# Optimization experiments

Hardware: AMD Instinct MI355X
Metric: run time of the kernel (lower is better)

## Reference

```python
import jax, jax.numpy as jnp
import numpy as np

B, K, P, N, COEF_D = 32, 2, 256, 8192, 10  # batch, parts, kp-per-part, cloud points
BETA = 0.1
SEP_FACTOR = 8.0
W_CHF, W_COV, W_SURF, W_JOINT, W_REG, W_SEP = 1.0, 1.0, 5.0, 1.0, 0.01, 2.0
# separation-loss pair indices (static, same as torch buffers select1/select2)
SEL1 = np.tile(np.arange(P), P - 1)
SEL2 = np.concatenate([np.arange(j, j + P) % P for j in range(1, P)])


def _pdist(a, b):
    # a: (..., M, 3), b: (..., N, 3) -> (..., M, N) euclidean distances
    d2 = (jnp.sum(a * a, -1)[..., :, None] + jnp.sum(b * b, -1)[..., None, :]
          - 2.0 * jnp.einsum('...mc,...nc->...mn', a, b))
    return jnp.sqrt(jnp.maximum(d2, 1e-12))


def _smooth_l1(pred, target, beta=BETA):
    d = jnp.abs(pred - target)
    return jnp.where(d < beta, 0.5 * d * d / beta, d - 0.5 * beta)


def setup_inputs() -> dict:
    key = jax.random.key(0)
    ks = jax.random.split(key, 10)
    return {
        'coefs': jax.random.normal(ks[0], (B, K * P, COEF_D), jnp.float32),
        'part_pred_kps': jax.random.normal(ks[1], (B, K, P, 3), jnp.float32),
        'part_nodes': jax.random.normal(ks[2], (B, K, P, 3), jnp.float32),
        'cloud': jax.random.normal(ks[3], (B, N, 3), jnp.float32),
        'cloud_cls': jax.random.randint(ks[4], (B, N), 0, K, jnp.int64),
        'pred_joint_loc': jax.random.normal(ks[5], (B, K - 1, 3), jnp.float32),
        'pred_joint_axis': jax.random.normal(ks[6], (B, K - 1, 3), jnp.float32),
        'gt_joint_loc': jax.random.normal(ks[7], (B, K - 1, 3), jnp.float32),
        'gt_joint_axis': jax.random.normal(ks[8], (B, K - 1, 3), jnp.float32),
        'gt_part_scale': jax.random.uniform(ks[9], (B, K, 3), jnp.float32),
    }


def _forward(coefs, part_pred_kps, part_nodes, cloud,
             pred_joint_loc, pred_joint_axis, gt_joint_loc, gt_joint_axis,
             gt_part_scale, cloud_cls):
    # ---- part chamfer (brute) over all parts at once: (B,K,M,N) ----
    d_chf = _pdist(part_pred_kps, part_nodes)
    fwd = jnp.min(d_chf, axis=3).mean(axis=(0, 2))   # (K,)
    bwd = jnp.min(d_chf, axis=2).mean(axis=(0, 2))   # (K,)
    chf_loss = jnp.mean(fwd + bwd)

    # ---- coverage loss: masked per-part pc extremes vs node extremes ----
    mask = cloud_cls[:, None, :] == jnp.arange(K)[None, :, None]  # (B,K,N)
    big = jnp.float32(1e9)
    pc = cloud[:, None, :, :]                                      # (B,1,N,3)
    pc_max = jnp.max(jnp.where(mask[..., None], pc, -big), axis=2)  # (B,K,3)
    pc_min = jnp.min(jnp.where(mask[..., None], pc, big), axis=2)
    kp_max = jnp.max(part_nodes, axis=2)                            # (B,K,3)
    kp_min = jnp.min(part_nodes, axis=2)
    cov_loss = jnp.mean((_smooth_l1(kp_max, pc_max) + _smooth_l1(kp_min, pc_min)) * 0.5)

    # ---- separation loss ----
    a = part_nodes[:, :, SEL1, :]
    b = part_nodes[:, :, SEL2, :]
    dist_sep = jnp.linalg.norm(a - b, axis=-1)                      # (B,K,L)
    thr = (jnp.linalg.norm(gt_part_scale, axis=-1) / SEP_FACTOR)[:, :, None]
    sep_loss = jnp.mean(jnp.maximum(0.0, thr - dist_sep))

    # ---- surface loss: single-side chamfer nodes -> cloud ----
    nodes = part_nodes.reshape(B, K * P, 3)
    d_surf = _pdist(nodes, cloud)                                   # (B, K*P, N)
    surf_loss = jnp.min(d_surf, axis=2).mean()

    # ---- joint loss ----
    dot = jnp.sum(pred_joint_axis * gt_joint_axis, -1)
    na = jnp.linalg.norm(pred_joint_axis, axis=-1)
    nb = jnp.linalg.norm(gt_joint_axis, axis=-1)
    loss_axis = 1.0 - (dot / jnp.maximum(na * nb, 1e-8)).mean()
    ngt = gt_joint_axis / jnp.linalg.norm(gt_joint_axis, axis=-1, keepdims=True)
    p = gt_joint_loc
    q = gt_joint_loc + ngt
    r = pred_joint_loc
    x = p - q
    t = jnp.sum((r - q) * x, -1, keepdims=True) / jnp.sum(x * x, -1, keepdims=True)
    loss_loc = jnp.linalg.norm(t * (p - q) + (q - r), axis=-1).mean()
    joint_loss = loss_loc * 1.0 + loss_axis * 0.5  # revolute: loc_weight=1, axis_weight=0.5

    reg_loss = jnp.mean(coefs * coefs)

    return (chf_loss * W_CHF + cov_loss * W_COV + surf_loss * W_SURF
            + joint_loss * W_JOINT + reg_loss * W_REG + sep_loss * W_SEP)


def reference(coefs, part_pred_kps, part_nodes, cloud, cloud_cls,
              pred_joint_loc, pred_joint_axis, gt_joint_loc, gt_joint_axis,
              gt_part_scale):
    return _forward(coefs, part_pred_kps, part_nodes, cloud,
                    pred_joint_loc, pred_joint_axis, gt_joint_loc,
                    gt_joint_axis, gt_part_scale, cloud_cls)
```

## Files before the change

kernel.cpp:

```cpp
#include <hip/hip_runtime.h>
#include <math.h>

#define NB 32
#define KK 2
#define PP 256
#define NCLOUD 8192
#define NNODES 512
#define NCOEF 163840
#define SURF0 193
#define NCHUNK 16
#define NSURF (NB * NCHUNK)
#define NBLK (SURF0 + NSURF)

#define SL_CHF 0
#define SL_SEP 64
#define SL_COV 128
#define SL_REG 192
#define SL_JNT 256
#define SL_SB 258
#define PART0 320

__device__ inline float waveSum(float v) {
#pragma unroll
  for (int o = 32; o > 0; o >>= 1) v += __shfl_down(v, o);
  return v;
}
__device__ inline float waveMax(float v) {
#pragma unroll
  for (int o = 32; o > 0; o >>= 1) v = fmaxf(v, __shfl_down(v, o));
  return v;
}
__device__ inline float waveMin(float v) {
#pragma unroll
  for (int o = 32; o > 0; o >>= 1) v = fminf(v, __shfl_down(v, o));
  return v;
}
__device__ inline float smooth_l1(float d) {
  d = fabsf(d);
  return d < 0.1f ? 5.0f * d * d : d - 0.05f;
}

__global__ __launch_bounds__(256) void mega_kernel(
    const float* __restrict__ coefs,
    const float* __restrict__ preds,
    const float* __restrict__ nodes,
    const float* __restrict__ cloud,
    const int* __restrict__ cls,
    const float* __restrict__ pjl, const float* __restrict__ pja,
    const float* __restrict__ gjl, const float* __restrict__ gja,
    const float* __restrict__ gps,
    float* __restrict__ ws) {
  const int bid = blockIdx.x;
  const int t = threadIdx.x;
  const int wave = t >> 6, lane = t & 63;
  __shared__ float4 sh4[512];
  __shared__ float shg[2048];
  __shared__ float red[12][4];

  if (bid < 64) {
    const int bk = bid;
    const float* pb = preds + (size_t)bk * PP * 3;
    const float* nbp = nodes + (size_t)bk * PP * 3;
    {
      float x = pb[3 * t], y = pb[3 * t + 1], z = pb[3 * t + 2];
      sh4[t] = make_float4(x, y, z, x * x + y * y + z * z);
      x = nbp[3 * t]; y = nbp[3 * t + 1]; z = nbp[3 * t + 2];
      sh4[256 + t] = make_float4(x, y, z, x * x + y * y + z * z);
    }
    __syncthreads();
    float4 ptv[4], ntv[4];
#pragma unroll
    for (int q = 0; q < 4; ++q) {
      ptv[q] = sh4[lane + q * 64];
      ntv[q] = sh4[256 + lane + q * 64];
    }
    const float s0 = gps[bk * 3 + 0], s1 = gps[bk * 3 + 1], s2 = gps[bk * 3 + 2];
    const float thr = sqrtf(s0 * s0 + s1 * s1 + s2 * s2) * 0.125f;
    float g1[4], g2[4], sep = 0.0f;
#pragma unroll
    for (int q = 0; q < 4; ++q) { g1[q] = 1e30f; g2[q] = 1e30f; }
    const int j0 = wave * 64;
#pragma unroll 2
    for (int jj = 0; jj < 64; ++jj) {
      const int j = j0 + jj;
      const float4 pj = sh4[j];
      const float4 nj = sh4[256 + j];
#pragma unroll
      for (int q = 0; q < 4; ++q) {
        float dot = fmaf(ptv[q].x, nj.x, fmaf(ptv[q].y, nj.y, ptv[q].z * nj.z));
        g1[q] = fminf(g1[q], fmaf(-2.0f, dot, nj.w));
        dot = fmaf(ntv[q].x, pj.x, fmaf(ntv[q].y, pj.y, ntv[q].z * pj.z));
        g2[q] = fminf(g2[q], fmaf(-2.0f, dot, pj.w));
        dot = fmaf(ntv[q].x, nj.x, fmaf(ntv[q].y, nj.y, ntv[q].z * nj.z));
        const float d2 = fmaf(-2.0f, dot, ntv[q].w + nj.w);
        const float d = sqrtf(fmaxf(d2, 0.0f));
        if (j != lane + q * 64) sep += fmaxf(thr - d, 0.0f);
      }
    }
#pragma unroll
    for (int q = 0; q < 4; ++q) {
      shg[wave * 256 + lane + q * 64] = g1[q];
      shg[1024 + wave * 256 + lane + q * 64] = g2[q];
    }
    __syncthreads();
    const float gf = fminf(fminf(shg[t], shg[256 + t]),
                           fminf(shg[512 + t], shg[768 + t]));
    const float gb = fminf(fminf(shg[1024 + t], shg[1280 + t]),
                           fminf(shg[1536 + t], shg[1792 + t]));
    float chf = sqrtf(fmaxf(sh4[t].w + gf, 1e-12f)) +
                sqrtf(fmaxf(sh4[256 + t].w + gb, 1e-12f));
    chf = waveSum(chf);
    sep = waveSum(sep);
    if (lane == 0) { red[0][wave] = chf; red[1][wave] = sep; }
    __syncthreads();
    if (t == 0) {
      ws[SL_CHF + bid] = red[0][0] + red[0][1] + red[0][2] + red[0][3];
      ws[SL_SEP + bid] = red[1][0] + red[1][1] + red[1][2] + red[1][3];
    }

  } else if (bid < 128) {
    const int bk = bid - 64;
    const int b = bk >> 1;
    const int k = bk & 1;
    float pmax0 = -1e9f, pmax1 = -1e9f, pmax2 = -1e9f;
    float pmin0 = 1e9f, pmin1 = 1e9f, pmin2 = 1e9f;
    const float* cb = cloud + (size_t)b * NCLOUD * 3;
    const int* lb = cls + (size_t)b * NCLOUD;
    for (int i = t; i < NCLOUD; i += 256) {
      if (lb[i] == k) {
        const float x = cb[i * 3 + 0], y = cb[i * 3 + 1], z = cb[i * 3 + 2];
        pmax0 = fmaxf(pmax0, x); pmax1 = fmaxf(pmax1, y); pmax2 = fmaxf(pmax2, z);
        pmin0 = fminf(pmin0, x); pmin1 = fminf(pmin1, y); pmin2 = fminf(pmin2, z);
      }
    }
    const float* nb = nodes + (size_t)bk * PP * 3;
    const float kx = nb[t * 3 + 0], ky = nb[t * 3 + 1], kz = nb[t * 3 + 2];
    pmax0 = waveMax(pmax0); pmax1 = waveMax(pmax1); pmax2 = waveMax(pmax2);
    pmin0 = waveMin(pmin0); pmin1 = waveMin(pmin1); pmin2 = waveMin(pmin2);
    float kmax0 = waveMax(kx), kmax1 = waveMax(ky), kmax2 = waveMax(kz);
    float kmin0 = waveMin(kx), kmin1 = waveMin(ky), kmin2 = waveMin(kz);
    if (lane == 0) {
      red[0][wave] = pmax0; red[1][wave] = pmax1; red[2][wave] = pmax2;
      red[3][wave] = pmin0; red[4][wave] = pmin1; red[5][wave] = pmin2;
      red[6][wave] = kmax0; red[7][wave] = kmax1; red[8][wave] = kmax2;
      red[9][wave] = kmin0; red[10][wave] = kmin1; red[11][wave] = kmin2;
    }
    __syncthreads();
    if (t == 0) {
      float v[12];
#pragma unroll
      for (int q = 0; q < 12; ++q) {
        if (q < 3 || (q >= 6 && q < 9))
          v[q] = fmaxf(fmaxf(red[q][0], red[q][1]), fmaxf(red[q][2], red[q][3]));
        else
          v[q] = fminf(fminf(red[q][0], red[q][1]), fminf(red[q][2], red[q][3]));
      }
      float s = 0.0f;
#pragma unroll
      for (int c2 = 0; c2 < 3; ++c2)
        s += 0.5f * (smooth_l1(v[6 + c2] - v[0 + c2]) + smooth_l1(v[9 + c2] - v[3 + c2]));
      ws[SL_COV + bk] = s;
    }

  } else if (bid < 192) {
    const int r = bid - 128;
    const float4* c4 = (const float4*)coefs;
    float v = 0.0f;
    for (int i = r * 256 + t; i < NCOEF / 4; i += 64 * 256) {
      const float4 q = c4[i];
      v += q.x * q.x + q.y * q.y + q.z * q.z + q.w * q.w;
    }
    v = waveSum(v);
    if (lane == 0) red[0][wave] = v;
    __syncthreads();
    if (t == 0)
      ws[SL_REG + r] = red[0][0] + red[0][1] + red[0][2] + red[0][3];

  } else if (bid == 192) {
    float cosv = 0.0f, locv = 0.0f;
    if (t < NB) {
      const float axj = pja[t * 3 + 0], ayj = pja[t * 3 + 1], azj = pja[t * 3 + 2];
      const float gx = gja[t * 3 + 0], gy = gja[t * 3 + 1], gz = gja[t * 3 + 2];
      const float dot = axj * gx + ayj * gy + azj * gz;
      const float na = sqrtf(axj * axj + ayj * ayj + azj * azj);
      const float nbn = sqrtf(gx * gx + gy * gy + gz * gz);
      cosv = dot / fmaxf(na * nbn, 1e-8f);
      const float ux = gx / nbn, uy = gy / nbn, uz = gz / nbn;
      const float px = gjl[t * 3 + 0], py = gjl[t * 3 + 1], pz = gjl[t * 3 + 2];
      const float qx = px + ux, qy = py + uy, qz = pz + uz;
      const float rx = pjl[t * 3 + 0], ry = pjl[t * 3 + 1], rz = pjl[t * 3 + 2];
      const float xx = px - qx, xy = py - qy, xz = pz - qz;
      const float tnum = (rx - qx) * xx + (ry - qy) * xy + (rz - qz) * xz;
      const float tden = xx * xx + xy * xy + xz * xz;
      const float tv = tnum / tden;
      const float vx = tv * xx + (qx - rx);
      const float vy = tv * xy + (qy - ry);
      const float vz = tv * xz + (qz - rz);
      locv = sqrtf(vx * vx + vy * vy + vz * vz);
    }
    cosv = waveSum(cosv);
    locv = waveSum(locv);
    if (t == 0) { ws[SL_JNT + 0] = cosv; ws[SL_JNT + 1] = locv; }

  } else {
    const int s = bid - SURF0;
    const int b = s >> 4;
    const int c = s & 15;
    const float* cb = cloud + ((size_t)b * NCLOUD + (size_t)c * 512) * 3;
#pragma unroll
    for (int g = 0; g < 2; ++g) {
      const int idx = g * 256 + t;
      const float qx = cb[3 * idx], qy = cb[3 * idx + 1], qz = cb[3 * idx + 2];
      sh4[idx] = make_float4(qx, qy, qz, 0.5f * (qx * qx + qy * qy + qz * qz));
    }
    __syncthreads();
    const float* nb = nodes + (size_t)b * NNODES * 3;
    float nxv[8], nyv[8], nzv[8], mg[8];
#pragma unroll
    for (int q = 0; q < 8; ++q) {
      const int n = lane + q * 64;
      nxv[q] = nb[3 * n]; nyv[q] = nb[3 * n + 1]; nzv[q] = nb[3 * n + 2];
      mg[q] = 1e30f;
    }
    const int p0 = wave * 128;
#pragma unroll 4
    for (int j = 0; j < 128; ++j) {
      const float4 q4 = sh4[p0 + j];
#pragma unroll
      for (int q = 0; q < 8; ++q)
        mg[q] = fminf(mg[q],
                      fmaf(-nxv[q], q4.x,
                           fmaf(-nyv[q], q4.y, fmaf(-nzv[q], q4.z, q4.w))));
    }
#pragma unroll
    for (int q = 0; q < 8; ++q)
      shg[wave * 512 + lane + q * 64] = mg[q];
    __syncthreads();
    float* pout = ws + PART0 + ((size_t)b * NCHUNK + c) * NNODES;
#pragma unroll
    for (int g = 0; g < 2; ++g) {
      const int node = g * 256 + t;
      pout[node] = fminf(fminf(shg[node], shg[512 + node]),
                         fminf(shg[1024 + node], shg[1536 + node]));
    }
  }
}

__global__ __launch_bounds__(256) void final1_kernel(
    const float* __restrict__ nodes, float* __restrict__ ws) {
  const int b = blockIdx.x;
  const int t = threadIdx.x;
  const float* partial = ws + PART0;
  const float* nb = nodes + (size_t)b * NNODES * 3;
  float ssum = 0.0f;
#pragma unroll
  for (int g = 0; g < 2; ++g) {
    const int node = g * 256 + t;
    float m = 1e30f;
#pragma unroll
    for (int c = 0; c < NCHUNK; ++c)
      m = fminf(m, partial[((size_t)b * NCHUNK + c) * NNODES + node]);
    const float x = nb[3 * node], y = nb[3 * node + 1], z = nb[3 * node + 2];
    const float nn = x * x + y * y + z * z;
    ssum += sqrtf(fmaxf(fmaf(2.0f, m, nn), 1e-12f));
  }
  ssum = waveSum(ssum);
  __shared__ float r[4];
  const int wave = t >> 6, lane = t & 63;
  if (lane == 0) r[wave] = ssum;
  __syncthreads();
  if (t == 0) ws[SL_SB + b] = r[0] + r[1] + r[2] + r[3];
}

__global__ __launch_bounds__(64) void final2_kernel(
    const float* __restrict__ ws, float* __restrict__ out) {
  const int t = threadIdx.x;
  float chf_s = ws[SL_CHF + t];
  float sep_s = ws[SL_SEP + t];
  float cov_s = ws[SL_COV + t];
  float reg_s = ws[SL_REG + t];
  float srf_s = (t < NB) ? ws[SL_SB + t] : 0.0f;
  chf_s = waveSum(chf_s);
  sep_s = waveSum(sep_s);
  cov_s = waveSum(cov_s);
  reg_s = waveSum(reg_s);
  srf_s = waveSum(srf_s);
  if (t == 0) {
    const float chf = chf_s / (float)(KK * NB * PP);
    const float sep = sep_s / (float)(NB * KK * PP * (PP - 1));
    const float surf = srf_s / (float)(NB * NNODES);
    const float cov = cov_s / (float)(NB * KK * 3);
    const float axis = 1.0f - ws[SL_JNT + 0] / (float)NB;
    const float loc = ws[SL_JNT + 1] / (float)NB;
    const float reg = reg_s / (float)NCOEF;
    out[0] = chf + cov + surf * 5.0f + (loc + 0.5f * axis) + reg * 0.01f + sep * 2.0f;
  }
}

extern "C" void kernel_launch(void* const* d_in, const int* in_sizes, int n_in,
                              void* d_out, int out_size, void* d_ws, size_t ws_size,
                              hipStream_t stream) {
  const float* coefs = (const float*)d_in[0];
  const float* preds = (const float*)d_in[1];
  const float* nodes = (const float*)d_in[2];
  const float* cloud = (const float*)d_in[3];
  const int* cls = (const int*)d_in[4];
  const float* pjl = (const float*)d_in[5];
  const float* pja = (const float*)d_in[6];
  const float* gjl = (const float*)d_in[7];
  const float* gja = (const float*)d_in[8];
  const float* gps = (const float*)d_in[9];
  float* out = (float*)d_out;
  float* ws = (float*)d_ws;

  mega_kernel<<<NBLK, 256, 0, stream>>>(coefs, preds, nodes, cloud, cls,
                                        pjl, pja, gjl, gja, gps, ws);
  final1_kernel<<<NB, 256, 0, stream>>>(nodes, ws);
  final2_kernel<<<1, 64, 0, stream>>>(ws, out);
}
```

Measured before the change: 29.50 us.

## Split chamfer and surface blocks finer and merge final reductions via atomicAdd

Chamfer/separation blocks now split the j range in half, giving twice as many blocks, and write per-half min partials that the final kernel combines. Surface blocks process 256-point chunks instead of 512, doubling the block count. The two finalisation kernels are merged into one that atomically adds per-batch contributions into the output, which is zeroed with a memset. This trades a kernel launch for a memset plus more workspace traffic, and makes the floating-point summation order nondeterministic.

```diff
diff --git a/kernel.cpp b/kernel.cpp
--- a/kernel.cpp
+++ b/kernel.cpp
@@ -7,18 +7,17 @@
 #define NCLOUD 8192
 #define NNODES 512
 #define NCOEF 163840
-#define SURF0 193
-#define NCHUNK 16
+#define SURF0 257
+#define NCHUNK 32
 #define NSURF (NB * NCHUNK)
 #define NBLK (SURF0 + NSURF)
 
-#define SL_CHF 0
-#define SL_SEP 64
+#define SL_SEP 0
 #define SL_COV 128
 #define SL_REG 192
 #define SL_JNT 256
-#define SL_SB 258
-#define PART0 320
+#define PCHF 288
+#define PART0 65824
 
 __device__ inline float waveSum(float v) {
 #pragma unroll
@@ -57,8 +56,9 @@
   __shared__ float shg[2048];
   __shared__ float red[12][4];
 
-  if (bid < 64) {
-    const int bk = bid;
+  if (bid < 128) {
+    const int bk = bid >> 1;
+    const int h = bid & 1;
     const float* pb = preds + (size_t)bk * PP * 3;
     const float* nbp = nodes + (size_t)bk * PP * 3;
     {
@@ -79,9 +79,9 @@
     float g1[4], g2[4], sep = 0.0f;
 #pragma unroll
     for (int q = 0; q < 4; ++q) { g1[q] = 1e30f; g2[q] = 1e30f; }
-    const int j0 = wave * 64;
+    const int j0 = h * 128 + wave * 32;
 #pragma unroll 2
-    for (int jj = 0; jj < 64; ++jj) {
+    for (int jj = 0; jj < 32; ++jj) {
       const int j = j0 + jj;
       const float4 pj = sh4[j];
       const float4 nj = sh4[256 + j];
@@ -99,27 +99,23 @@
     }
 #pragma unroll
     for (int q = 0; q < 4; ++q) {
-      shg[wave * 256 + lane + q * 64] = g1[q];
-      shg[1024 + wave * 256 + lane + q * 64] = g2[q];
-    }
-    __syncthreads();
-    const float gf = fminf(fminf(shg[t], shg[256 + t]),
-                           fminf(shg[512 + t], shg[768 + t]));
-    const float gb = fminf(fminf(shg[1024 + t], shg[1280 + t]),
-                           fminf(shg[1536 + t], shg[1792 + t]));
-    float chf = sqrtf(fmaxf(sh4[t].w + gf, 1e-12f)) +
-                sqrtf(fmaxf(sh4[256 + t].w + gb, 1e-12f));
-    chf = waveSum(chf);
+      shg[wave * 256 + lane + q * 64] = ptv[q].w + g1[q];
+      shg[1024 + wave * 256 + lane + q * 64] = ntv[q].w + g2[q];
+    }
+    __syncthreads();
+    float* pc = ws + PCHF + (size_t)bid * 512;
+    pc[t] = fminf(fminf(shg[t], shg[256 + t]),
+                  fminf(shg[512 + t], shg[768 + t]));
+    pc[256 + t] = fminf(fminf(shg[1024 + t], shg[1280 + t]),
+                        fminf(shg[1536 + t], shg[1792 + t]));
     sep = waveSum(sep);
-    if (lane == 0) { red[0][wave] = chf; red[1][wave] = sep; }
-    __syncthreads();
-    if (t == 0) {
-      ws[SL_CHF + bid] = red[0][0] + red[0][1] + red[0][2] + red[0][3];
-      ws[SL_SEP + bid] = red[1][0] + red[1][1] + red[1][2] + red[1][3];
-    }
-
-  } else if (bid < 128) {
-    const int bk = bid - 64;
+    if (lane == 0) red[0][wave] = sep;
+    __syncthreads();
+    if (t == 0)
+      ws[SL_SEP + bid] = red[0][0] + red[0][1] + red[0][2] + red[0][3];
+
+  } else if (bid < 192) {
+    const int bk = bid - 128;
     const int b = bk >> 1;
     const int k = bk & 1;
     float pmax0 = -1e9f, pmax1 = -1e9f, pmax2 = -1e9f;
@@ -162,8 +158,8 @@
       ws[SL_COV + bk] = s;
     }
 
-  } else if (bid < 192) {
-    const int r = bid - 128;
+  } else if (bid < 256) {
+    const int r = bid - 192;
     const float4* c4 = (const float4*)coefs;
     float v = 0.0f;
     for (int i = r * 256 + t; i < NCOEF / 4; i += 64 * 256) {
@@ -176,7 +172,7 @@
     if (t == 0)
       ws[SL_REG + r] = red[0][0] + red[0][1] + red[0][2] + red[0][3];
 
-  } else if (bid == 192) {
+  } else if (bid == 256) {
     float cosv = 0.0f, locv = 0.0f;
     if (t < NB) {
       const float axj = pja[t * 3 + 0], ayj = pja[t * 3 + 1], azj = pja[t * 3 + 2];
@@ -204,14 +200,12 @@
 
   } else {
     const int s = bid - SURF0;
-    const int b = s >> 4;
-    const int c = s & 15;
-    const float* cb = cloud + ((size_t)b * NCLOUD + (size_t)c * 512) * 3;
-#pragma unroll
-    for (int g = 0; g < 2; ++g) {
-      const int idx = g * 256 + t;
-      const float qx = cb[3 * idx], qy = cb[3 * idx + 1], qz = cb[3 * idx + 2];
-      sh4[idx] = make_float4(qx, qy, qz, 0.5f * (qx * qx + qy * qy + qz * qz));
+    const int b = s >> 5;
+    const int c = s & 31;
+    const float* cb = cloud + ((size_t)b * NCLOUD + (size_t)c * 256) * 3;
+    {
+      const float qx = cb[3 * t], qy = cb[3 * t + 1], qz = cb[3 * t + 2];
+      sh4[t] = make_float4(qx, qy, qz, 0.5f * (qx * qx + qy * qy + qz * qz));
     }
     __syncthreads();
     const float* nb = nodes + (size_t)b * NNODES * 3;
@@ -222,9 +216,9 @@
       nxv[q] = nb[3 * n]; nyv[q] = nb[3 * n + 1]; nzv[q] = nb[3 * n + 2];
       mg[q] = 1e30f;
     }
-    const int p0 = wave * 128;
+    const int p0 = wave * 64;
 #pragma unroll 4
-    for (int j = 0; j < 128; ++j) {
+    for (int j = 0; j < 64; ++j) {
       const float4 q4 = sh4[p0 + j];
 #pragma unroll
       for (int q = 0; q < 8; ++q)
@@ -247,9 +241,11 @@
 }
 
 __global__ __launch_bounds__(256) void final1_kernel(
-    const float* __restrict__ nodes, float* __restrict__ ws) {
+    const float* __restrict__ nodes, const float* __restrict__ ws,
+    float* __restrict__ out) {
   const int b = blockIdx.x;
   const int t = threadIdx.x;
+  const int wave = t >> 6, lane = t & 63;
   const float* partial = ws + PART0;
   const float* nb = nodes + (size_t)b * NNODES * 3;
   float ssum = 0.0f;
@@ -264,36 +260,38 @@
     const float nn = x * x + y * y + z * z;
     ssum += sqrtf(fmaxf(fmaf(2.0f, m, nn), 1e-12f));
   }
+  float csum = 0.0f;
+#pragma unroll
+  for (int k = 0; k < KK; ++k) {
+    const int bk = b * KK + k;
+    const float* h0 = ws + PCHF + (size_t)(2 * bk) * 512;
+    const float* h1 = ws + PCHF + (size_t)(2 * bk + 1) * 512;
+    const float fwd = fminf(h0[t], h1[t]);
+    const float bwd = fminf(h0[256 + t], h1[256 + t]);
+    csum += sqrtf(fmaxf(fwd, 1e-12f)) + sqrtf(fmaxf(bwd, 1e-12f));
+  }
   ssum = waveSum(ssum);
-  __shared__ float r[4];
-  const int wave = t >> 6, lane = t & 63;
-  if (lane == 0) r[wave] = ssum;
+  csum = waveSum(csum);
+  __shared__ float r[2][4];
+  if (lane == 0) { r[0][wave] = ssum; r[1][wave] = csum; }
   __syncthreads();
-  if (t == 0) ws[SL_SB + b] = r[0] + r[1] + r[2] + r[3];
-}
-
-__global__ __launch_bounds__(64) void final2_kernel(
-    const float* __restrict__ ws, float* __restrict__ out) {
-  const int t = threadIdx.x;
-  float chf_s = ws[SL_CHF + t];
-  float sep_s = ws[SL_SEP + t];
-  float cov_s = ws[SL_COV + t];
-  float reg_s = ws[SL_REG + t];
-  float srf_s = (t < NB) ? ws[SL_SB + t] : 0.0f;
-  chf_s = waveSum(chf_s);
-  sep_s = waveSum(sep_s);
-  cov_s = waveSum(cov_s);
-  reg_s = waveSum(reg_s);
-  srf_s = waveSum(srf_s);
   if (t == 0) {
-    const float chf = chf_s / (float)(KK * NB * PP);
-    const float sep = sep_s / (float)(NB * KK * PP * (PP - 1));
-    const float surf = srf_s / (float)(NB * NNODES);
-    const float cov = cov_s / (float)(NB * KK * 3);
-    const float axis = 1.0f - ws[SL_JNT + 0] / (float)NB;
-    const float loc = ws[SL_JNT + 1] / (float)NB;
-    const float reg = reg_s / (float)NCOEF;
-    out[0] = chf + cov + surf * 5.0f + (loc + 0.5f * axis) + reg * 0.01f + sep * 2.0f;
+    const float ssum_t = r[0][0] + r[0][1] + r[0][2] + r[0][3];
+    const float csum_t = r[1][0] + r[1][1] + r[1][2] + r[1][3];
+    float v = ssum_t * (5.0f / (float)(NB * NNODES)) +
+              csum_t * (1.0f / (float)(KK * NB * PP));
+    v += (ws[SL_COV + 2 * b] + ws[SL_COV + 2 * b + 1]) *
+         (1.0f / (float)(NB * KK * 3));
+    v += (ws[SL_REG + 2 * b] + ws[SL_REG + 2 * b + 1]) * (0.01f / (float)NCOEF);
+    v += (ws[SL_SEP + 4 * b] + ws[SL_SEP + 4 * b + 1] + ws[SL_SEP + 4 * b + 2] +
+          ws[SL_SEP + 4 * b + 3]) *
+         (2.0f / (float)(NB * KK * PP * (PP - 1)));
+    if (b == 0) {
+      const float axis = 1.0f - ws[SL_JNT + 0] / (float)NB;
+      const float loc = ws[SL_JNT + 1] / (float)NB;
+      v += loc + 0.5f * axis;
+    }
+    atomicAdd(out, v);
   }
 }
 
@@ -313,8 +311,8 @@
   float* out = (float*)d_out;
   float* ws = (float*)d_ws;
 
+  hipMemsetAsync(out, 0, sizeof(float), stream);
   mega_kernel<<<NBLK, 256, 0, stream>>>(coefs, preds, nodes, cloud, cls,
                                         pjl, pja, gjl, gja, gps, ws);
-  final1_kernel<<<NB, 256, 0, stream>>>(nodes, ws);
-  final2_kernel<<<1, 64, 0, stream>>>(ws, out);
-}
+  final1_kernel<<<NB, 256, 0, stream>>>(nodes, ws, out);
+}
```

New measurement: 30.88 us. 1.05x slower.

## Split chamfer/separation blocks four ways per part and merge partial minima later

Applied to the files above, without the earlier changes.

Each (batch,part) chamfer+separation block is split into four blocks, each scanning a quarter of the j range. The blocks write per-point partial minima (with the squared norm already added) to workspace, and final1_kernel merges them and does the sqrt/sum. The aim is to shorten the critical path of the O(P^2) chamfer work by giving it four times the parallelism. In exchange it adds workspace traffic, redundant shared-memory loads per block, and more blocks competing with the surface blocks.

```diff
diff --git a/kernel.cpp b/kernel.cpp
--- a/kernel.cpp
+++ b/kernel.cpp
@@ -7,18 +7,19 @@
 #define NCLOUD 8192
 #define NNODES 512
 #define NCOEF 163840
-#define SURF0 193
+#define SURF0 385
 #define NCHUNK 16
 #define NSURF (NB * NCHUNK)
 #define NBLK (SURF0 + NSURF)
 
-#define SL_CHF 0
-#define SL_SEP 64
-#define SL_COV 128
-#define SL_REG 192
-#define SL_JNT 256
-#define SL_SB 258
-#define PART0 320
+#define SL_SEP 0
+#define SL_COV 256
+#define SL_REG 320
+#define SL_JNT 384
+#define SL_SB 386
+#define SL_CB 418
+#define PCHF 512
+#define PART0 131584
 
 __device__ inline float waveSum(float v) {
 #pragma unroll
@@ -57,8 +58,9 @@
   __shared__ float shg[2048];
   __shared__ float red[12][4];
 
-  if (bid < 64) {
-    const int bk = bid;
+  if (bid < 256) {
+    const int bk = bid >> 2;
+    const int h = bid & 3;
     const float* pb = preds + (size_t)bk * PP * 3;
     const float* nbp = nodes + (size_t)bk * PP * 3;
     {
@@ -79,9 +81,9 @@
     float g1[4], g2[4], sep = 0.0f;
 #pragma unroll
     for (int q = 0; q < 4; ++q) { g1[q] = 1e30f; g2[q] = 1e30f; }
-    const int j0 = wave * 64;
-#pragma unroll 2
-    for (int jj = 0; jj < 64; ++jj) {
+    const int j0 = h * 64 + wave * 16;
+#pragma unroll 4
+    for (int jj = 0; jj < 16; ++jj) {
       const int j = j0 + jj;
       const float4 pj = sh4[j];
       const float4 nj = sh4[256 + j];
@@ -99,27 +101,23 @@
     }
 #pragma unroll
     for (int q = 0; q < 4; ++q) {
-      shg[wave * 256 + lane + q * 64] = g1[q];
-      shg[1024 + wave * 256 + lane + q * 64] = g2[q];
-    }
-    __syncthreads();
-    const float gf = fminf(fminf(shg[t], shg[256 + t]),
-                           fminf(shg[512 + t], shg[768 + t]));
-    const float gb = fminf(fminf(shg[1024 + t], shg[1280 + t]),
-                           fminf(shg[1536 + t], shg[1792 + t]));
-    float chf = sqrtf(fmaxf(sh4[t].w + gf, 1e-12f)) +
-                sqrtf(fmaxf(sh4[256 + t].w + gb, 1e-12f));
-    chf = waveSum(chf);
+      shg[wave * 256 + lane + q * 64] = ptv[q].w + g1[q];
+      shg[1024 + wave * 256 + lane + q * 64] = ntv[q].w + g2[q];
+    }
+    __syncthreads();
+    float* pc = ws + PCHF + (size_t)bid * 512;
+    pc[t] = fminf(fminf(shg[t], shg[256 + t]),
+                  fminf(shg[512 + t], shg[768 + t]));
+    pc[256 + t] = fminf(fminf(shg[1024 + t], shg[1280 + t]),
+                        fminf(shg[1536 + t], shg[1792 + t]));
     sep = waveSum(sep);
-    if (lane == 0) { red[0][wave] = chf; red[1][wave] = sep; }
-    __syncthreads();
-    if (t == 0) {
-      ws[SL_CHF + bid] = red[0][0] + red[0][1] + red[0][2] + red[0][3];
-      ws[SL_SEP + bid] = red[1][0] + red[1][1] + red[1][2] + red[1][3];
-    }
-
-  } else if (bid < 128) {
-    const int bk = bid - 64;
+    if (lane == 0) red[0][wave] = sep;
+    __syncthreads();
+    if (t == 0)
+      ws[SL_SEP + bid] = red[0][0] + red[0][1] + red[0][2] + red[0][3];
+
+  } else if (bid < 320) {
+    const int bk = bid - 256;
     const int b = bk >> 1;
     const int k = bk & 1;
     float pmax0 = -1e9f, pmax1 = -1e9f, pmax2 = -1e9f;
@@ -162,8 +160,8 @@
       ws[SL_COV + bk] = s;
     }
 
-  } else if (bid < 192) {
-    const int r = bid - 128;
+  } else if (bid < 384) {
+    const int r = bid - 320;
     const float4* c4 = (const float4*)coefs;
     float v = 0.0f;
     for (int i = r * 256 + t; i < NCOEF / 4; i += 64 * 256) {
@@ -176,7 +174,7 @@
     if (t == 0)
       ws[SL_REG + r] = red[0][0] + red[0][1] + red[0][2] + red[0][3];
 
-  } else if (bid == 192) {
+  } else if (bid == 384) {
     float cosv = 0.0f, locv = 0.0f;
     if (t < NB) {
       const float axj = pja[t * 3 + 0], ayj = pja[t * 3 + 1], azj = pja[t * 3 + 2];
@@ -250,6 +248,7 @@
     const float* __restrict__ nodes, float* __restrict__ ws) {
   const int b = blockIdx.x;
   const int t = threadIdx.x;
+  const int wave = t >> 6, lane = t & 63;
   const float* partial = ws + PART0;
   const float* nb = nodes + (size_t)b * NNODES * 3;
   float ssum = 0.0f;
@@ -264,27 +263,44 @@
     const float nn = x * x + y * y + z * z;
     ssum += sqrtf(fmaxf(fmaf(2.0f, m, nn), 1e-12f));
   }
+  float csum = 0.0f;
+#pragma unroll
+  for (int k = 0; k < KK; ++k) {
+    const int bk = b * KK + k;
+    const float* q0 = ws + PCHF + (size_t)(4 * bk + 0) * 512;
+    const float* q1 = ws + PCHF + (size_t)(4 * bk + 1) * 512;
+    const float* q2 = ws + PCHF + (size_t)(4 * bk + 2) * 512;
+    const float* q3 = ws + PCHF + (size_t)(4 * bk + 3) * 512;
+    const float fwd = fminf(fminf(q0[t], q1[t]), fminf(q2[t], q3[t]));
+    const float bwd = fminf(fminf(q0[256 + t], q1[256 + t]),
+                            fminf(q2[256 + t], q3[256 + t]));
+    csum += sqrtf(fmaxf(fwd, 1e-12f)) + sqrtf(fmaxf(bwd, 1e-12f));
+  }
   ssum = waveSum(ssum);
-  __shared__ float r[4];
-  const int wave = t >> 6, lane = t & 63;
-  if (lane == 0) r[wave] = ssum;
+  csum = waveSum(csum);
+  __shared__ float r[2][4];
+  if (lane == 0) { r[0][wave] = ssum; r[1][wave] = csum; }
   __syncthreads();
-  if (t == 0) ws[SL_SB + b] = r[0] + r[1] + r[2] + r[3];
+  if (t == 0) {
+    ws[SL_SB + b] = r[0][0] + r[0][1] + r[0][2] + r[0][3];
+    ws[SL_CB + b] = r[1][0] + r[1][1] + r[1][2] + r[1][3];
+  }
 }
 
 __global__ __launch_bounds__(64) void final2_kernel(
     const float* __restrict__ ws, float* __restrict__ out) {
   const int t = threadIdx.x;
-  float chf_s = ws[SL_CHF + t];
-  float sep_s = ws[SL_SEP + t];
+  float sep_s = ws[SL_SEP + t] + ws[SL_SEP + 64 + t] + ws[SL_SEP + 128 + t] +
+                ws[SL_SEP + 192 + t];
   float cov_s = ws[SL_COV + t];
   float reg_s = ws[SL_REG + t];
   float srf_s = (t < NB) ? ws[SL_SB + t] : 0.0f;
-  chf_s = waveSum(chf_s);
+  float chf_s = (t < NB) ? ws[SL_CB + t] : 0.0f;
   sep_s = waveSum(sep_s);
   cov_s = waveSum(cov_s);
   reg_s = waveSum(reg_s);
   srf_s = waveSum(srf_s);
+  chf_s = waveSum(chf_s);
   if (t == 0) {
     const float chf = chf_s / (float)(KK * NB * PP);
     const float sep = sep_s / (float)(NB * KK * PP * (PP - 1));
```

New measurement: 26.06 us. 1.13x faster.
